# Kernel tuning notes

Hardware: AMD Instinct MI355X
Metric: run time of the kernel (lower is better)

Reference implementation:

```python
import jax, jax.numpy as jnp
import numpy as np

B, T, C, P = 512, 365, 10, 64  # batch, num_steps, input_dim, num_prototypes


def setup_inputs() -> dict:
    key = jax.random.key(0)
    k1, k2, k3, k4 = jax.random.split(key, 4)
    input_seq = jax.random.normal(k1, (B, T, C), dtype=jnp.float32)
    # binary observation mask (some dates missing)
    mask = (jax.random.uniform(k2, (B, T)) > 0.1).astype(jnp.float32)
    label = jax.random.randint(k3, (B,), 0, P)
    prototypes = jax.random.normal(k4, (P, T, C), dtype=jnp.float32)
    return {"input_seq": input_seq, "mask": mask, "label": label,
            "prototypes": prototypes}


def reference(input_seq, mask, label, prototypes):
    # distances[b,p] = sum_{t,c} mask[b,t] * (x[b,t,c] - proto[p,t,c])^2
    # expanded so we never materialize the [B,P,T,C] broadcast:
    #   = sum mask*x^2  - 2*sum mask*x*p + sum mask*p^2
    x2 = jnp.einsum('btc,btc,bt->b', input_seq, input_seq, mask)          # [B]
    xp = jnp.einsum('btc,bt,ptc->bp', input_seq, mask, prototypes)        # [B,P]
    p2 = jnp.einsum('bt,ptc,ptc->bp', mask, prototypes, prototypes)       # [B,P]
    distances = x2[:, None] - 2.0 * xp + p2                               # [B,P]
    indices = jnp.argmin(distances, axis=1)                               # [B]
    # gather selected prototype per sample (trans/offset inactive -> shared protos)
    output_seq = prototypes[indices]                                      # [B,T,C]
    return (output_seq, input_seq, distances, indices, label, mask)
```

## Files before the change

kernel.cpp:

```cpp
#include <hip/hip_runtime.h>

#define B_  512
#define T_  365
#define C_  10
#define P_  64
#define K_  3650
#define K2_ 1825
#define KP_ 3712

#define OFF_OUT0 0u
#define OFF_IN   1868800u
#define OFF_DIST 3737600u
#define OFF_IDX  3770368u
#define OFF_LAB  3770880u
#define OFF_MASK 3771392u

__global__ __launch_bounds__(1024) void dist_kernel(
    const float* __restrict__ x, const float* __restrict__ mask,
    const int* __restrict__ label, const float* __restrict__ protos,
    float* __restrict__ out)
{
    __shared__ float xm[2][KP_];
    __shared__ float mexp[2][KP_];
    __shared__ float mrow[2][368];
    __shared__ float dist[2][64];
    __shared__ int   sel[2];

    const int tid  = threadIdx.x;
    const int lane = tid & 63;
    const int wv   = tid >> 6;
    const int b0   = blockIdx.x * 2;

    if (tid < T_)                    mrow[0][tid] = mask[(size_t)b0 * T_ + tid];
    {
        int t2 = tid - 512;
        if (t2 >= 0 && t2 < T_)      mrow[1][t2] = mask[(size_t)(b0 + 1) * T_ + t2];
    }
    __syncthreads();

    for (int i = tid; i < KP_; i += 1024) {
#pragma unroll
        for (int bb = 0; bb < 2; ++bb) {
            float m = 0.f, v = 0.f;
            if (i < K_) {
                m = mrow[bb][i / C_];
                v = x[(size_t)(b0 + bb) * K_ + i] * m;
            }
            xm[bb][i]   = v;
            mexp[bb][i] = m;
        }
    }
    __syncthreads();

    const int p0 = wv * 4;
    const float2* pr[4];
#pragma unroll
    for (int q = 0; q < 4; ++q)
        pr[q] = (const float2*)(protos + (size_t)(p0 + q) * K_);
    const float2* xr0 = (const float2*)&xm[0][0];
    const float2* xr1 = (const float2*)&xm[1][0];
    const float2* mr0 = (const float2*)&mexp[0][0];
    const float2* mr1 = (const float2*)&mexp[1][0];

    float acc0[4] = {0.f, 0.f, 0.f, 0.f};
    float acc1[4] = {0.f, 0.f, 0.f, 0.f};

#pragma unroll 2
    for (int it = 0; it < 29; ++it) {
        const int i2  = it * 64 + lane;
        const int i2c = i2 < K2_ ? i2 : (K2_ - 1);
        float2 pv[4];
#pragma unroll
        for (int q = 0; q < 4; ++q) pv[q] = pr[q][i2c];
        const float2 u0 = xr0[i2], m0 = mr0[i2];
        const float2 u1 = xr1[i2], m1 = mr1[i2];
#pragma unroll
        for (int q = 0; q < 4; ++q) {
            float tx, ty;
            tx = fmaf(-pv[q].x, m0.x, u0.x); acc0[q] = fmaf(tx, tx, acc0[q]);
            ty = fmaf(-pv[q].y, m0.y, u0.y); acc0[q] = fmaf(ty, ty, acc0[q]);
            tx = fmaf(-pv[q].x, m1.x, u1.x); acc1[q] = fmaf(tx, tx, acc1[q]);
            ty = fmaf(-pv[q].y, m1.y, u1.y); acc1[q] = fmaf(ty, ty, acc1[q]);
        }
    }

#pragma unroll
    for (int q = 0; q < 4; ++q) {
        float v0 = acc0[q], v1 = acc1[q];
        for (int off = 32; off; off >>= 1) {
            v0 += __shfl_down(v0, off);
            v1 += __shfl_down(v1, off);
        }
        if (lane == 0) {
            dist[0][p0 + q] = v0;
            dist[1][p0 + q] = v1;
        }
    }
    __syncthreads();

    if (tid < 128) {
        int bb = tid >> 6;
        out[OFF_DIST + (size_t)(b0 + bb) * P_ + lane] = dist[bb][lane];
    }
    if (wv < 2) {
        const int bb = wv;
        float v = dist[bb][lane];
        int idx = lane;
        for (int off = 32; off; off >>= 1) {
            float ov = __shfl_down(v, off);
            int   oi = __shfl_down(idx, off);
            if (ov < v || (ov == v && oi < idx)) { v = ov; idx = oi; }
        }
        if (lane == 0) {
            sel[bb] = idx;
            const int b = b0 + bb;
            out[OFF_IDX + b] = (float)idx;
            out[OFF_LAB + b] = (float)label[b];
        }
    }
    __syncthreads();

#pragma unroll
    for (int bb = 0; bb < 2; ++bb) {
        const float2* src = (const float2*)(protos + (size_t)sel[bb] * K_);
        float2* dst = (float2*)(out + OFF_OUT0 + (size_t)(b0 + bb) * K_);
        for (int i2 = tid; i2 < K2_; i2 += 1024) dst[i2] = src[i2];
    }
}

extern "C" void kernel_launch(void* const* d_in, const int* in_sizes, int n_in,
                              void* d_out, int out_size, void* d_ws, size_t ws_size,
                              hipStream_t stream) {
    const float* x      = (const float*)d_in[0];
    const float* mask   = (const float*)d_in[1];
    const int*   label  = (const int*)d_in[2];
    const float* protos = (const float*)d_in[3];
    float* out = (float*)d_out;

    hipMemcpyAsync(out + OFF_IN,   x,    (size_t)B_ * K_ * sizeof(float),
                   hipMemcpyDeviceToDevice, stream);
    hipMemcpyAsync(out + OFF_MASK, mask, (size_t)B_ * T_ * sizeof(float),
                   hipMemcpyDeviceToDevice, stream);

    dist_kernel<<<B_ / 2, 1024, 0, stream>>>(x, mask, label, protos, out);
}
```

Baseline: 90.60 us.

## Fold passthrough copies into distance kernel and split argmin/gather into second kernel

Removes the two device-to-device memcpy calls and has the distance kernel write the input and mask passthrough outputs while it loads them. The distance work is split across two blocks per sample pair, each handling 32 prototypes with 512 threads, to raise block count and occupancy. Argmin and the prototype gather move to a separate per-sample kernel that reads distances from global memory. In exchange, each sample pair's x and mask are loaded twice, and there is an extra kernel launch plus a global round trip for the distances.

```diff
diff --git a/kernel.cpp b/kernel.cpp
--- a/kernel.cpp
+++ b/kernel.cpp
@@ -1,12 +1,13 @@
 #include <hip/hip_runtime.h>
 
-#define B_  512
-#define T_  365
-#define C_  10
-#define P_  64
-#define K_  3650
-#define K2_ 1825
-#define KP_ 3712
+#define B_   512
+#define T_   365
+#define C_   10
+#define P_   64
+#define K_   3650
+#define K2_  1825
+#define KP_  3712
+#define KP2_ 1856
 
 #define OFF_OUT0 0u
 #define OFF_IN   1868800u
@@ -15,44 +16,54 @@
 #define OFF_LAB  3770880u
 #define OFF_MASK 3771392u
 
-__global__ __launch_bounds__(1024) void dist_kernel(
+__global__ __launch_bounds__(512, 4) void dist_kernel(
     const float* __restrict__ x, const float* __restrict__ mask,
-    const int* __restrict__ label, const float* __restrict__ protos,
-    float* __restrict__ out)
+    const float* __restrict__ protos, float* __restrict__ out)
 {
     __shared__ float xm[2][KP_];
     __shared__ float mexp[2][KP_];
     __shared__ float mrow[2][368];
-    __shared__ float dist[2][64];
-    __shared__ int   sel[2];
 
     const int tid  = threadIdx.x;
     const int lane = tid & 63;
     const int wv   = tid >> 6;
-    const int b0   = blockIdx.x * 2;
+    const int bp   = blockIdx.x >> 1;
+    const int ph   = blockIdx.x & 1;
+    const int b0   = bp * 2;
 
-    if (tid < T_)                    mrow[0][tid] = mask[(size_t)b0 * T_ + tid];
-    {
-        int t2 = tid - 512;
-        if (t2 >= 0 && t2 < T_)      mrow[1][t2] = mask[(size_t)(b0 + 1) * T_ + t2];
+    for (int t = tid; t < 2 * T_; t += 512) {
+        int bb = t >= T_;
+        int tt = t - bb * T_;
+        float m = mask[(size_t)(b0 + bb) * T_ + tt];
+        mrow[bb][tt] = m;
+        if (ph == 0) out[OFF_MASK + (size_t)(b0 + bb) * T_ + tt] = m;
     }
     __syncthreads();
 
-    for (int i = tid; i < KP_; i += 1024) {
 #pragma unroll
-        for (int bb = 0; bb < 2; ++bb) {
-            float m = 0.f, v = 0.f;
-            if (i < K_) {
-                m = mrow[bb][i / C_];
-                v = x[(size_t)(b0 + bb) * K_ + i] * m;
+    for (int bb = 0; bb < 2; ++bb) {
+        const float2* xr = (const float2*)(x + (size_t)(b0 + bb) * K_);
+        float2*       er = (float2*)(out + OFF_IN + (size_t)(b0 + bb) * K_);
+        float2*       sx = (float2*)&xm[bb][0];
+        float2*       sm = (float2*)&mexp[bb][0];
+        for (int i2 = tid; i2 < KP2_; i2 += 512) {
+            float2 v = {0.f, 0.f}, mm = {0.f, 0.f};
+            if (i2 < K2_) {
+                v = xr[i2];
+                if (ph == 0) er[i2] = v;
+                int e = i2 * 2;
+                mm.x = mrow[bb][e / C_];
+                mm.y = mrow[bb][(e + 1) / C_];
+                v.x *= mm.x;
+                v.y *= mm.y;
             }
-            xm[bb][i]   = v;
-            mexp[bb][i] = m;
+            sx[i2] = v;
+            sm[i2] = mm;
         }
     }
     __syncthreads();
 
-    const int p0 = wv * 4;
+    const int p0 = ph * 32 + wv * 4;
     const float2* pr[4];
 #pragma unroll
     for (int q = 0; q < 4; ++q)
@@ -65,7 +76,7 @@
     float acc0[4] = {0.f, 0.f, 0.f, 0.f};
     float acc1[4] = {0.f, 0.f, 0.f, 0.f};
 
-#pragma unroll 2
+#pragma unroll 4
     for (int it = 0; it < 29; ++it) {
         const int i2  = it * 64 + lane;
         const int i2c = i2 < K2_ ? i2 : (K2_ - 1);
@@ -92,19 +103,23 @@
             v1 += __shfl_down(v1, off);
         }
         if (lane == 0) {
-            dist[0][p0 + q] = v0;
-            dist[1][p0 + q] = v1;
+            out[OFF_DIST + (size_t)b0 * P_ + p0 + q]       = v0;
+            out[OFF_DIST + (size_t)(b0 + 1) * P_ + p0 + q] = v1;
         }
     }
-    __syncthreads();
+}
 
-    if (tid < 128) {
-        int bb = tid >> 6;
-        out[OFF_DIST + (size_t)(b0 + bb) * P_ + lane] = dist[bb][lane];
-    }
-    if (wv < 2) {
-        const int bb = wv;
-        float v = dist[bb][lane];
+__global__ __launch_bounds__(256) void argmin_kernel(
+    const int* __restrict__ label, const float* __restrict__ protos,
+    float* __restrict__ out)
+{
+    __shared__ int sel;
+    const int b    = blockIdx.x;
+    const int tid  = threadIdx.x;
+    const int lane = tid & 63;
+
+    if (tid < 64) {
+        float v = out[OFF_DIST + (size_t)b * P_ + lane];
         int idx = lane;
         for (int off = 32; off; off >>= 1) {
             float ov = __shfl_down(v, off);
@@ -112,20 +127,16 @@
             if (ov < v || (ov == v && oi < idx)) { v = ov; idx = oi; }
         }
         if (lane == 0) {
-            sel[bb] = idx;
-            const int b = b0 + bb;
+            sel = idx;
             out[OFF_IDX + b] = (float)idx;
             out[OFF_LAB + b] = (float)label[b];
         }
     }
     __syncthreads();
 
-#pragma unroll
-    for (int bb = 0; bb < 2; ++bb) {
-        const float2* src = (const float2*)(protos + (size_t)sel[bb] * K_);
-        float2* dst = (float2*)(out + OFF_OUT0 + (size_t)(b0 + bb) * K_);
-        for (int i2 = tid; i2 < K2_; i2 += 1024) dst[i2] = src[i2];
-    }
+    const float2* src = (const float2*)(protos + (size_t)sel * K_);
+    float2* dst = (float2*)(out + OFF_OUT0 + (size_t)b * K_);
+    for (int i2 = tid; i2 < K2_; i2 += 256) dst[i2] = src[i2];
 }
 
 extern "C" void kernel_launch(void* const* d_in, const int* in_sizes, int n_in,
@@ -137,10 +148,6 @@
     const float* protos = (const float*)d_in[3];
     float* out = (float*)d_out;
 
-    hipMemcpyAsync(out + OFF_IN,   x,    (size_t)B_ * K_ * sizeof(float),
-                   hipMemcpyDeviceToDevice, stream);
-    hipMemcpyAsync(out + OFF_MASK, mask, (size_t)B_ * T_ * sizeof(float),
-                   hipMemcpyDeviceToDevice, stream);
-
-    dist_kernel<<<B_ / 2, 1024, 0, stream>>>(x, mask, label, protos, out);
+    dist_kernel<<<512, 512, 0, stream>>>(x, mask, protos, out);
+    argmin_kernel<<<B_, 256, 0, stream>>>(label, protos, out);
 }
```

New measurement: 90.37 us. About the same (-0.3%).
